# Kernel optimization log

Measured on AMD Instinct MI355X. Metric: run time of the kernel, lower is better.

Reference implementation:

```python
import jax, jax.numpy as jnp
import numpy as np

H = 8          # kv heads
D = 128        # head dim
EPS = 1e-6
NEG = -1e9

def rmsnorm(x, w):
    rms = jnp.sqrt(jnp.mean(x * x, axis=-1, keepdims=True) + EPS)
    return x / rms * w

def apply_rotary(x, cos, sin):
    # x: [B, h, T, D]; cos/sin: [1, 1, T, D/2]
    x1, x2 = jnp.split(x, 2, axis=-1)
    return jnp.concatenate([x1 * cos - x2 * sin, x1 * sin + x2 * cos], axis=-1)


def setup_inputs() -> dict:
    key = jax.random.key(0)
    ks = jax.random.split(key, 7)
    B, T, hid = 1, 4096, 1024
    s = 0.02
    return {
        "x":   jax.random.normal(ks[0], (B, T, hid), jnp.float32),
        "cos": jax.random.normal(ks[1], (1, 1, T, D // 2), jnp.float32),
        "sin": jax.random.normal(ks[2], (1, 1, T, D // 2), jnp.float32),
        "Wq":  jax.random.normal(ks[3], (hid, 2 * hid), jnp.float32) * s,
        "Wk":  jax.random.normal(ks[4], (hid, hid), jnp.float32) * s,
        "Wv":  jax.random.normal(ks[5], (hid, hid), jnp.float32) * s,
        "Wo":  jax.random.normal(ks[6], (2 * hid, hid), jnp.float32) * s,
        "qn_w": jnp.ones((D,), jnp.float32),
        "kn_w": jnp.ones((D,), jnp.float32),
    }


def reference(x, cos, sin, Wq, Wk, Wv, Wo, qn_w, kn_w):
    B, T, _ = x.shape
    scale = D ** -0.5

    q = (x @ Wq).reshape(B, T, 2 * H, D).transpose(0, 2, 1, 3)  # [B,2H,T,D]
    k = (x @ Wk).reshape(B, T, H, D).transpose(0, 2, 1, 3)      # [B,H,T,D]
    v = (x @ Wv).reshape(B, T, H, D).transpose(0, 2, 1, 3)      # [B,H,T,D]

    q = apply_rotary(rmsnorm(q, qn_w), cos, sin)
    k = apply_rotary(rmsnorm(k, kn_w), cos, sin)

    # GQA expand: query head i uses kv head i // 2
    k = jnp.repeat(k, 2, axis=1)  # [B,2H,T,D]
    v = jnp.repeat(v, 2, axis=1)

    attn = jnp.einsum("bhtd,bhsd->bhts", q, k) * scale
    causal = jnp.tril(jnp.ones((T, T), bool))
    attn = jnp.where(causal, attn, NEG)
    attn = jax.nn.softmax(attn, axis=-1)

    out = jnp.einsum("bhts,bhsd->bhtd", attn, v)
    out = out.transpose(0, 2, 1, 3).reshape(B, T, 2 * H * D)
    return out @ Wo
```

## Files before the change

### kernel.cpp

```cpp
#include <hip/hip_runtime.h>
#include <hip/hip_bf16.h>

#define H2 16
#define HKV 8
#define DHEAD 128
#define HID 1024
#define NQ 2048

typedef unsigned short u16;
typedef __bf16 bf16x8 __attribute__((ext_vector_type(8)));
typedef float f32x4 __attribute__((ext_vector_type(4)));

__device__ __forceinline__ u16 f2bf(float x) {
    unsigned int u = __float_as_uint(x);
    unsigned int r = (u + 0x7fffu + ((u >> 16) & 1u)) >> 16;
    return (u16)r;
}
__device__ __forceinline__ float bf2f(u16 x) {
    return __uint_as_float(((unsigned int)x) << 16);
}

__device__ __forceinline__ unsigned int pack_bf16(float hi, float lo) {
    unsigned int a = __float_as_uint(hi) + 0x8000u;
    unsigned int b = __float_as_uint(lo) + 0x8000u;
    return __builtin_amdgcn_perm(a, b, 0x07060302u);
}

__device__ __forceinline__ bf16x8 ld_frag(const u16* p) {
    bf16x8 r;
    *reinterpret_cast<uint4*>(&r) = *reinterpret_cast<const uint4*>(p);
    return r;
}

__device__ __forceinline__ void gload_lds16(const u16* g, u16* l) {
    __builtin_amdgcn_global_load_lds((const __attribute__((address_space(1))) void*)g,
                                     (__attribute__((address_space(3))) void*)l, 16, 0, 0);
}

__global__ __launch_bounds__(256) void cast_f32_bf16(const float* __restrict__ in,
                                                     u16* __restrict__ out, int n4) {
    int i = blockIdx.x * 256 + threadIdx.x;
    if (i < n4) {
        float4 v = reinterpret_cast<const float4*>(in)[i];
        ushort4 o;
        o.x = f2bf(v.x); o.y = f2bf(v.y); o.z = f2bf(v.z); o.w = f2bf(v.w);
        reinterpret_cast<ushort4*>(out)[i] = o;
    }
}

__global__ __launch_bounds__(256) void transpose_cast_all(const float* __restrict__ Wq,
                                                          const float* __restrict__ Wk,
                                                          const float* __restrict__ Wv,
                                                          const float* __restrict__ Wo,
                                                          u16* __restrict__ Wqkvb,
                                                          u16* __restrict__ Wob) {
    __shared__ u16 t[32][34];
    int bid = blockIdx.x;
    const float* in; u16* out; int K, N, k0, n0;
    if (bid < 2048) {
        in = Wq; out = Wqkvb; K = 1024; N = 2048;
        k0 = (bid & 31) * 32; n0 = (bid >> 5) * 32;
    } else if (bid < 3072) {
        int b = bid - 2048;
        in = Wk; out = Wqkvb + (size_t)2048 * 1024; K = 1024; N = 1024;
        k0 = (b & 31) * 32; n0 = (b >> 5) * 32;
    } else if (bid < 4096) {
        int b = bid - 3072;
        in = Wv; out = Wqkvb + (size_t)3072 * 1024; K = 1024; N = 1024;
        k0 = (b & 31) * 32; n0 = (b >> 5) * 32;
    } else {
        int b = bid - 4096;
        in = Wo; out = Wob; K = 2048; N = 1024;
        k0 = (b & 63) * 32; n0 = (b >> 6) * 32;
    }
    for (int c = threadIdx.x; c < 1024; c += 256) {
        int k = c >> 5, n = c & 31;
        t[k][n] = f2bf(in[(size_t)(k0 + k) * N + n0 + n]);
    }
    __syncthreads();
    for (int c = threadIdx.x; c < 1024; c += 256) {
        int n = c >> 5, k = c & 31;
        out[(size_t)(n0 + n) * K + k0 + k] = t[k][n];
    }
}

template <bool OUT_BF16>
__global__ __launch_bounds__(256) void gemm_bf16_t(const u16* __restrict__ A,
                                                   const u16* __restrict__ Bt,
                                                   void* __restrict__ Cv,
                                                   int M, int N, int K) {
    __shared__ u16 As[2][128 * 32];
    __shared__ u16 Bs[2][128 * 32];
    int tid = threadIdx.x;
    int lane = tid & 63, wave = tid >> 6;
    int quad = lane >> 4, l15 = lane & 15;
    int wr = wave >> 1, wc = wave & 1;
    int m0 = blockIdx.y * 128, n0 = blockIdx.x * 128;

    f32x4 zero = {0.f, 0.f, 0.f, 0.f};
    f32x4 acc[4][4];
    for (int i = 0; i < 4; i++)
        for (int j = 0; j < 4; j++) acc[i][j] = zero;

    int r0 = 16 * wave + (lane >> 2);
    int r1 = r0 + 64;
    int ks0 = (lane & 3) ^ ((r0 >> 1) & 3);
    int ks1 = (lane & 3) ^ ((r1 >> 1) & 3);
    const u16* ga0 = A + (size_t)(m0 + r0) * K + ks0 * 8;
    const u16* ga1 = A + (size_t)(m0 + r1) * K + ks1 * 8;
    const u16* gb0 = Bt + (size_t)(n0 + r0) * K + ks0 * 8;
    const u16* gb1 = Bt + (size_t)(n0 + r1) * K + ks1 * 8;

    int swz = (quad ^ ((l15 >> 1) & 3)) * 8;

    for (int k0 = 0; k0 < K; k0 += 64) {
        __syncthreads();
        #pragma unroll
        for (int s = 0; s < 2; s++) {
            gload_lds16(ga0 + k0 + s * 32, &As[s][wave * 512]);
            gload_lds16(ga1 + k0 + s * 32, &As[s][(wave + 4) * 512]);
            gload_lds16(gb0 + k0 + s * 32, &Bs[s][wave * 512]);
            gload_lds16(gb1 + k0 + s * 32, &Bs[s][(wave + 4) * 512]);
        }
        __syncthreads();
        #pragma unroll
        for (int s = 0; s < 2; s++) {
            bf16x8 a[4], b[4];
            #pragma unroll
            for (int i = 0; i < 4; i++) a[i] = ld_frag(&As[s][(64 * wr + 16 * i + l15) * 32 + swz]);
            #pragma unroll
            for (int j = 0; j < 4; j++) b[j] = ld_frag(&Bs[s][(64 * wc + 16 * j + l15) * 32 + swz]);
            #pragma unroll
            for (int i = 0; i < 4; i++)
                #pragma unroll
                for (int j = 0; j < 4; j++)
                    acc[i][j] = __builtin_amdgcn_mfma_f32_16x16x32_bf16(a[i], b[j], acc[i][j], 0, 0, 0);
        }
    }
    for (int i = 0; i < 4; i++) {
        int rowb = m0 + 64 * wr + 16 * i + quad * 4;
        for (int j = 0; j < 4; j++) {
            int col = n0 + 64 * wc + 16 * j + l15;
            for (int r = 0; r < 4; r++) {
                if (OUT_BF16)
                    ((u16*)Cv)[(size_t)(rowb + r) * N + col] = f2bf(acc[i][j][r]);
                else
                    ((float*)Cv)[(size_t)(rowb + r) * N + col] = acc[i][j][r];
            }
        }
    }
}

__global__ __launch_bounds__(256) void gemm_bf16_n64(const u16* __restrict__ A,
                                                     const u16* __restrict__ Bt,
                                                     float* __restrict__ C,
                                                     int M, int N, int K) {
    __shared__ u16 As[2][128 * 32];
    __shared__ u16 Bs[2][64 * 32];
    int tid = threadIdx.x;
    int lane = tid & 63, wave = tid >> 6;
    int quad = lane >> 4, l15 = lane & 15;
    int m0 = blockIdx.y * 128, n0 = blockIdx.x * 64;

    f32x4 zero = {0.f, 0.f, 0.f, 0.f};
    f32x4 acc[2][4];
    for (int i = 0; i < 2; i++)
        for (int j = 0; j < 4; j++) acc[i][j] = zero;

    int ra0 = 32 * wave + (lane >> 2);
    int ra1 = ra0 + 16;
    int rb  = 16 * wave + (lane >> 2);
    int ksa0 = (lane & 3) ^ ((ra0 >> 1) & 3);
    int ksa1 = (lane & 3) ^ ((ra1 >> 1) & 3);
    int ksb  = (lane & 3) ^ ((rb >> 1) & 3);
    const u16* ga0 = A + (size_t)(m0 + ra0) * K + ksa0 * 8;
    const u16* ga1 = A + (size_t)(m0 + ra1) * K + ksa1 * 8;
    const u16* gb  = Bt + (size_t)(n0 + rb) * K + ksb * 8;

    int swz = (quad ^ ((l15 >> 1) & 3)) * 8;

    for (int k0 = 0; k0 < K; k0 += 64) {
        __syncthreads();
        #pragma unroll
        for (int s = 0; s < 2; s++) {
            gload_lds16(ga0 + k0 + s * 32, &As[s][(2 * wave) * 512]);
            gload_lds16(ga1 + k0 + s * 32, &As[s][(2 * wave + 1) * 512]);
            gload_lds16(gb + k0 + s * 32, &Bs[s][wave * 512]);
        }
        __syncthreads();
        #pragma unroll
        for (int s = 0; s < 2; s++) {
            bf16x8 a[2], b[4];
            #pragma unroll
            for (int i = 0; i < 2; i++) a[i] = ld_frag(&As[s][(32 * wave + 16 * i + l15) * 32 + swz]);
            #pragma unroll
            for (int j = 0; j < 4; j++) b[j] = ld_frag(&Bs[s][(16 * j + l15) * 32 + swz]);
            #pragma unroll
            for (int i = 0; i < 2; i++)
                #pragma unroll
                for (int j = 0; j < 4; j++)
                    acc[i][j] = __builtin_amdgcn_mfma_f32_16x16x32_bf16(a[i], b[j], acc[i][j], 0, 0, 0);
        }
    }
    for (int i = 0; i < 2; i++) {
        int rowb = m0 + 32 * wave + 16 * i + quad * 4;
        for (int j = 0; j < 4; j++) {
            int col = n0 + 16 * j + l15;
            for (int r = 0; r < 4; r++)
                C[(size_t)(rowb + r) * N + col] = acc[i][j][r];
        }
    }
}

__global__ __launch_bounds__(256) void norm_rope_qk(const u16* __restrict__ qkv,
                                                    const float* __restrict__ cosp,
                                                    const float* __restrict__ sinp,
                                                    const float* __restrict__ qnw,
                                                    const float* __restrict__ knw,
                                                    u16* __restrict__ Qb,
                                                    u16* __restrict__ Kb,
                                                    int T, float qscale) {
    int wave = threadIdx.x >> 6, lane = threadIdx.x & 63;
    int wid = blockIdx.x * 4 + wave;
    int t = wid / 24, unit = wid % 24;
    if (t >= T) return;
    bool isq = unit < 16;
    int coloff = isq ? unit * 128 : 2048 + (unit - 16) * 128;
    const float* w = isq ? qnw : knw;
    float outscale = isq ? qscale : 1.0f;
    u16* out = isq ? (Qb + ((size_t)unit * T + t) * 128)
                   : (Kb + ((size_t)(unit - 16) * T + t) * 128);
    const u16* r = qkv + (size_t)t * 4096 + coloff;
    float v1 = bf2f(r[lane]), v2 = bf2f(r[lane + 64]);
    float ss = v1 * v1 + v2 * v2;
    for (int off = 1; off < 64; off <<= 1) ss += __shfl_xor(ss, off);
    float inv = rsqrtf(ss * (1.f / 128.f) + 1e-6f);
    float n1 = v1 * inv * w[lane], n2 = v2 * inv * w[lane + 64];
    float c = cosp[(size_t)t * 64 + lane], s = sinp[(size_t)t * 64 + lane];
    float o1 = (n1 * c - n2 * s) * outscale;
    float o2 = (n1 * s + n2 * c) * outscale;
    out[lane] = f2bf(o1);
    out[lane + 64] = f2bf(o2);
}

__global__ __launch_bounds__(256) void v_transpose(const u16* __restrict__ qkv,
                                                   u16* __restrict__ Vbt, int T) {
    __shared__ u16 tt[128][72];
    int h = blockIdx.y, t0 = blockIdx.x * 64;
    for (int c = threadIdx.x; c < 8192; c += 256) {
        int r = c >> 7, d = c & 127;
        tt[d][r] = qkv[(size_t)(t0 + r) * 4096 + 3072 + h * 128 + d];
    }
    __syncthreads();
    for (int c = threadIdx.x; c < 8192; c += 256) {
        int d = c >> 6, r = c & 63;
        Vbt[((size_t)h * 128 + d) * T + t0 + r] = tt[d][r];
    }
}

__global__ __launch_bounds__(512, 4) void flash_attn(const u16* __restrict__ Qb,
                                                     const u16* __restrict__ Kb,
                                                     const u16* __restrict__ Vbt,
                                                     u16* __restrict__ attn, int T) {
    __shared__ u16 Ks[2][64 * 128];
    __shared__ u16 Vt[2][128 * 64];
    __shared__ u16 Ps[64 * 64];
    __shared__ float Ms[4][2][16];
    __shared__ float Ls[4][2][16];
    int tid = threadIdx.x;
    int lane = tid & 63, wave = tid >> 6;
    int qw = wave & 3, sh = wave >> 2;
    int quad = lane >> 4, l15 = lane & 15;
    int swb8 = (l15 & 7) * 8;
    int h = blockIdx.y;
    int j = (int)blockIdx.x;
    int kvh = h >> 1;

    const u16* kbase = Kb + (size_t)kvh * T * 128;
    const u16* vbase = Vbt + (size_t)kvh * 128 * T;

    int krow_ = lane >> 4;
    int kseg_ = lane & 15;
    int vrow_ = lane >> 3;
    int vseg_ = lane & 7;

    auto stage = [&](int s0, int b) {
        #pragma unroll
        for (int i = 0; i < 2; i++) {
            int ch = wave * 2 + i;
            int r = ch * 4 + krow_;
            int s = kseg_ ^ (r & 7);
            gload_lds16(kbase + (size_t)(s0 + r) * 128 + s * 8, &Ks[b][ch * 512]);
        }
        #pragma unroll
        for (int i = 0; i < 2; i++) {
            int ch = wave * 2 + i;
            int d = ch * 8 + vrow_;
            int s = vseg_ ^ (d & 7);
            gload_lds16(vbase + (size_t)d * T + s0 + s * 8, &Vt[b][ch * 512]);
        }
    };

    bf16x8 onesf;
    #pragma unroll
    for (int i = 0; i < 8; i++) onesf[i] = (__bf16)1.0f;
    f32x4 zero = {0.f, 0.f, 0.f, 0.f};
    const float L2E = 1.44269504f;

    for (int pass = 0; pass < 2; ++pass) {
        int qt = pass == 0 ? (63 - j) : j;
        int q0 = qt * 64;

        bf16x8 qf[4];
        {
            const u16* qp = Qb + ((size_t)h * T + q0 + 16 * qw + l15) * 128 + quad * 8;
            #pragma unroll
            for (int kk = 0; kk < 4; kk++) qf[kk] = ld_frag(qp + kk * 32);
        }

        float m_i = -3.0e38f;
        f32x4 lsum = zero;
        f32x4 o[8];
        for (int dt = 0; dt < 8; dt++) o[dt] = zero;

        int ntiles = qt + 1;
        stage(0, 0);
        __syncthreads();

        for (int it = 0; it < ntiles; ++it) {
            int b = it & 1;
            if (it + 1 < ntiles) stage((it + 1) * 64, 1 - b);
            bool diag = (it == qt);
            if (!(diag && sh == 1 && qw < 2)) {
                f32x4 scT[2];
                scT[0] = zero; scT[1] = zero;
                #pragma unroll
                for (int kk = 0; kk < 4; kk++)
                    #pragma unroll
                    for (int jt = 0; jt < 2; jt++) {
                        bf16x8 kfrag = ld_frag(&Ks[b][(sh * 32 + jt * 16 + l15) * 128 + ((kk * 32 + quad * 8) ^ swb8)]);
                        scT[jt] = __builtin_amdgcn_mfma_f32_16x16x32_bf16(kfrag, qf[kk], scT[jt], 0, 0, 0);
                    }

                if (diag) {
                    int qloc = 16 * qw + l15;
                    #pragma unroll
                    for (int jt = 0; jt < 2; jt++)
                        for (int r = 0; r < 4; r++)
                            if (sh * 32 + jt * 16 + quad * 4 + r > qloc) scT[jt][r] = -1e30f;
                }

                float mt = scT[0][0];
                #pragma unroll
                for (int jt = 0; jt < 2; jt++)
                    for (int r = 0; r < 4; r++) mt = fmaxf(mt, scT[jt][r]);
                mt = fmaxf(mt, __shfl_xor(mt, 16));
                mt = fmaxf(mt, __shfl_xor(mt, 32));
                float mnew = fmaxf(m_i, mt);
                float alpha = __expf(m_i - mnew);
                m_i = mnew;
                float mls = mnew * L2E;

                #pragma unroll
                for (int jt = 0; jt < 2; jt++)
                    for (int r = 0; r < 4; r++)
                        scT[jt][r] = exp2f(fmaf(scT[jt][r], L2E, -mls));

                {
                    int prow = 16 * qw + l15;
                    #pragma unroll
                    for (int jt = 0; jt < 2; jt++) {
                        int s8 = sh * 4 + 2 * jt + (quad >> 1);
                        uint2 wv;
                        wv.x = pack_bf16(scT[jt][1], scT[jt][0]);
                        wv.y = pack_bf16(scT[jt][3], scT[jt][2]);
                        *reinterpret_cast<uint2*>(&Ps[prow * 64 + (s8 ^ (l15 & 7)) * 8 + (quad & 1) * 4]) = wv;
                    }
                }

                if (__any(alpha != 1.0f)) {
                    float av[4];
                    #pragma unroll
                    for (int r = 0; r < 4; r++) av[r] = __shfl(alpha, quad * 4 + r);
                    #pragma unroll
                    for (int r = 0; r < 4; r++) lsum[r] *= av[r];
                    #pragma unroll
                    for (int dt = 0; dt < 8; dt++)
                        for (int r = 0; r < 4; r++) o[dt][r] *= av[r];
                }

                asm volatile("s_waitcnt lgkmcnt(0)" ::: "memory");

                bf16x8 pa = ld_frag(&Ps[(16 * qw + l15) * 64 + (((sh * 4 + quad) ^ (l15 & 7)) * 8)]);
                lsum = __builtin_amdgcn_mfma_f32_16x16x32_bf16(pa, onesf, lsum, 0, 0, 0);
                #pragma unroll
                for (int dt = 0; dt < 8; dt++) {
                    bf16x8 vb = ld_frag(&Vt[b][(dt * 16 + l15) * 64 + (((sh * 4 + quad) * 8) ^ swb8)]);
                    o[dt] = __builtin_amdgcn_mfma_f32_16x16x32_bf16(pa, vb, o[dt], 0, 0, 0);
                }
            }
            __syncthreads();
        }

        if (quad == 0) Ms[qw][sh][l15] = m_i;
        if (l15 == 0) {
            #pragma unroll
            for (int r = 0; r < 4; r++) Ls[qw][sh][quad * 4 + r] = lsum[r];
        }
        __syncthreads();
        float M4[4], wS[4];
        #pragma unroll
        for (int r = 0; r < 4; r++) {
            float mS = Ms[qw][sh][quad * 4 + r];
            float mO = Ms[qw][sh ^ 1][quad * 4 + r];
            M4[r] = fmaxf(mS, mO);
            wS[r] = __expf(mS - M4[r]);
        }
        float* scr = reinterpret_cast<float*>(&Ks[0][0]);
        if (sh == 1) {
            #pragma unroll
            for (int dt = 0; dt < 8; dt++)
                #pragma unroll
                for (int r = 0; r < 4; r++)
                    scr[qw * 2048 + (dt * 16 + l15) * 16 + ((quad * 4 + r) ^ l15)] = o[dt][r] * wS[r];
        }
        __syncthreads();
        if (sh == 0) {
            float inv[4];
            #pragma unroll
            for (int r = 0; r < 4; r++) {
                float mO = Ms[qw][1][quad * 4 + r];
                float wO = __expf(mO - M4[r]);
                float l = lsum[r] * wS[r] + Ls[qw][1][quad * 4 + r] * wO;
                inv[r] = 1.f / l;
            }
            #pragma unroll
            for (int dt = 0; dt < 8; dt++)
                #pragma unroll
                for (int r = 0; r < 4; r++) {
                    float val = (o[dt][r] * wS[r] +
                                 scr[qw * 2048 + (dt * 16 + l15) * 16 + ((quad * 4 + r) ^ l15)]) * inv[r];
                    int row = q0 + 16 * qw + quad * 4 + r;
                    attn[(size_t)row * NQ + h * DHEAD + dt * 16 + l15] = f2bf(val);
                }
        }
        __syncthreads();
    }
}

extern "C" void kernel_launch(void* const* d_in, const int* in_sizes, int n_in,
                              void* d_out, int out_size, void* d_ws, size_t ws_size,
                              hipStream_t stream) {
    const float* x    = (const float*)d_in[0];
    const float* cosp = (const float*)d_in[1];
    const float* sinp = (const float*)d_in[2];
    const float* Wq   = (const float*)d_in[3];
    const float* Wk   = (const float*)d_in[4];
    const float* Wv   = (const float*)d_in[5];
    const float* Wo   = (const float*)d_in[6];
    const float* qnw  = (const float*)d_in[7];
    const float* knw  = (const float*)d_in[8];
    float* out = (float*)d_out;
    const int T = in_sizes[1] / 64;

    char* ws = (char*)d_ws;
    size_t off = 0;
    auto alloc = [&](size_t bytes) {
        char* p = ws + off;
        off += (bytes + 255) & ~(size_t)255;
        return p;
    };
    u16*   xb     = (u16*)alloc((size_t)T * HID * 2);
    u16*   Wqkvb  = (u16*)alloc((size_t)4096 * HID * 2);
    u16*   Wob    = (u16*)alloc((size_t)HID * NQ * 2);
    u16*   qkvb   = (u16*)alloc((size_t)T * 4096 * 2);
    u16*   Qb     = (u16*)alloc((size_t)H2 * T * DHEAD * 2);
    u16*   Kb     = (u16*)alloc((size_t)HKV * T * DHEAD * 2);
    u16*   Vbt    = (u16*)alloc((size_t)HKV * DHEAD * T * 2);
    u16*   attn   = (u16*)alloc((size_t)T * NQ * 2);

    cast_f32_bf16<<<(T * HID / 4 + 255) / 256, 256, 0, stream>>>(x, xb, T * HID / 4);
    transpose_cast_all<<<6144, 256, 0, stream>>>(Wq, Wk, Wv, Wo, Wqkvb, Wob);

    gemm_bf16_t<true><<<dim3(4096 / 128, T / 128), 256, 0, stream>>>(xb, Wqkvb, qkvb, T, 4096, HID);

    const float scale = 0.08838834764831845f;
    norm_rope_qk<<<T * 24 / 4, 256, 0, stream>>>(qkvb, cosp, sinp, qnw, knw, Qb, Kb, T, scale);
    v_transpose<<<dim3(T / 64, HKV), 256, 0, stream>>>(qkvb, Vbt, T);

    flash_attn<<<dim3(32, H2), 512, 0, stream>>>(Qb, Kb, Vbt, attn, T);

    gemm_bf16_n64<<<dim3(HID / 64, T / 128), 256, 0, stream>>>(attn, Wob, out, T, HID, NQ);
}
```

Baseline: 354.3 us.

## Enlarge flash attention query tile to 128 rows per block

Each block now handles 128 query rows instead of 64, with each wave computing two 16-row query sub-tiles against the same K/V fragments. This doubles the reuse of every K and V tile staged into shared memory and halves the number of blocks. In exchange, register pressure roughly doubles (launch bounds drop to 2 blocks per CU), the grid shrinks to 256 blocks, and causal masking now runs over a two-tile diagonal zone.

```diff
diff --git a/kernel.cpp b/kernel.cpp
--- a/kernel.cpp
+++ b/kernel.cpp
@@ -258,22 +258,23 @@
     }
 }
 
-__global__ __launch_bounds__(512, 4) void flash_attn(const u16* __restrict__ Qb,
+__global__ __launch_bounds__(512, 2) void flash_attn(const u16* __restrict__ Qb,
                                                      const u16* __restrict__ Kb,
                                                      const u16* __restrict__ Vbt,
                                                      u16* __restrict__ attn, int T) {
     __shared__ u16 Ks[2][64 * 128];
     __shared__ u16 Vt[2][128 * 64];
-    __shared__ u16 Ps[64 * 64];
-    __shared__ float Ms[4][2][16];
-    __shared__ float Ls[4][2][16];
+    __shared__ u16 Ps[128 * 64];
+    __shared__ float Ms[4][2][32];
+    __shared__ float Ls[4][2][32];
     int tid = threadIdx.x;
     int lane = tid & 63, wave = tid >> 6;
     int qw = wave & 3, sh = wave >> 2;
     int quad = lane >> 4, l15 = lane & 15;
     int swb8 = (l15 & 7) * 8;
     int h = blockIdx.y;
-    int j = (int)blockIdx.x;
+    int jj = (int)blockIdx.x;
+    int nqt = T >> 7;
     int kvh = h >> 1;
 
     const u16* kbase = Kb + (size_t)kvh * T * 128;
@@ -308,141 +309,171 @@
     const float L2E = 1.44269504f;
 
     for (int pass = 0; pass < 2; ++pass) {
-        int qt = pass == 0 ? (63 - j) : j;
-        int q0 = qt * 64;
-
-        bf16x8 qf[4];
-        {
-            const u16* qp = Qb + ((size_t)h * T + q0 + 16 * qw + l15) * 128 + quad * 8;
-            #pragma unroll
-            for (int kk = 0; kk < 4; kk++) qf[kk] = ld_frag(qp + kk * 32);
-        }
-
-        float m_i = -3.0e38f;
-        f32x4 lsum = zero;
-        f32x4 o[8];
-        for (int dt = 0; dt < 8; dt++) o[dt] = zero;
-
-        int ntiles = qt + 1;
+        int qt = pass == 0 ? (nqt - 1 - jj) : jj;
+        int q0 = qt * 128;
+
+        bf16x8 qf[2][4];
+        #pragma unroll
+        for (int qs = 0; qs < 2; qs++) {
+            const u16* qp = Qb + ((size_t)h * T + q0 + 32 * qw + 16 * qs + l15) * 128 + quad * 8;
+            #pragma unroll
+            for (int kk = 0; kk < 4; kk++) qf[qs][kk] = ld_frag(qp + kk * 32);
+        }
+
+        float m_i[2] = {-3.0e38f, -3.0e38f};
+        f32x4 lsum[2] = {zero, zero};
+        f32x4 o[2][8];
+        #pragma unroll
+        for (int qs = 0; qs < 2; qs++)
+            #pragma unroll
+            for (int dt = 0; dt < 8; dt++) o[qs][dt] = zero;
+
+        int ntiles = 2 * qt + 2;
         stage(0, 0);
         __syncthreads();
 
         for (int it = 0; it < ntiles; ++it) {
             int b = it & 1;
             if (it + 1 < ntiles) stage((it + 1) * 64, 1 - b);
-            bool diag = (it == qt);
-            if (!(diag && sh == 1 && qw < 2)) {
-                f32x4 scT[2];
-                scT[0] = zero; scT[1] = zero;
+            bool diagzone = (it >= 2 * qt);
+            int sbl = (it - 2 * qt) * 64 + 32 * sh;
+            bool skip = diagzone && (32 * qw + 31 < sbl);
+            if (!skip) {
+                f32x4 scT[2][2];
+                scT[0][0] = zero; scT[0][1] = zero; scT[1][0] = zero; scT[1][1] = zero;
                 #pragma unroll
                 for (int kk = 0; kk < 4; kk++)
                     #pragma unroll
                     for (int jt = 0; jt < 2; jt++) {
-                        bf16x8 kfrag = ld_frag(&Ks[b][(sh * 32 + jt * 16 + l15) * 128 + ((kk * 32 + quad * 8) ^ swb8)]);
-                        scT[jt] = __builtin_amdgcn_mfma_f32_16x16x32_bf16(kfrag, qf[kk], scT[jt], 0, 0, 0);
+                        bf16x8 kfrag = ld_frag(&Ks[b][(32 * sh + 16 * jt + l15) * 128 + ((kk * 32 + quad * 8) ^ swb8)]);
+                        scT[0][jt] = __builtin_amdgcn_mfma_f32_16x16x32_bf16(kfrag, qf[0][kk], scT[0][jt], 0, 0, 0);
+                        scT[1][jt] = __builtin_amdgcn_mfma_f32_16x16x32_bf16(kfrag, qf[1][kk], scT[1][jt], 0, 0, 0);
                     }
 
-                if (diag) {
-                    int qloc = 16 * qw + l15;
+                if (diagzone) {
+                    #pragma unroll
+                    for (int qs = 0; qs < 2; qs++) {
+                        int qloc = 32 * qw + 16 * qs + l15;
+                        #pragma unroll
+                        for (int jt = 0; jt < 2; jt++)
+                            for (int r = 0; r < 4; r++)
+                                if (sbl + 16 * jt + quad * 4 + r > qloc) scT[qs][jt][r] = -1e30f;
+                    }
+                }
+
+                #pragma unroll
+                for (int qs = 0; qs < 2; qs++) {
+                    float mt = scT[qs][0][0];
+                    #pragma unroll
+                    for (int jt = 0; jt < 2; jt++)
+                        for (int r = 0; r < 4; r++) mt = fmaxf(mt, scT[qs][jt][r]);
+                    mt = fmaxf(mt, __shfl_xor(mt, 16));
+                    mt = fmaxf(mt, __shfl_xor(mt, 32));
+                    float mnew = fmaxf(m_i[qs], mt);
+                    float alpha = __expf(m_i[qs] - mnew);
+                    m_i[qs] = mnew;
+                    float mls = mnew * L2E;
+
                     #pragma unroll
                     for (int jt = 0; jt < 2; jt++)
                         for (int r = 0; r < 4; r++)
-                            if (sh * 32 + jt * 16 + quad * 4 + r > qloc) scT[jt][r] = -1e30f;
-                }
-
-                float mt = scT[0][0];
-                #pragma unroll
-                for (int jt = 0; jt < 2; jt++)
-                    for (int r = 0; r < 4; r++) mt = fmaxf(mt, scT[jt][r]);
-                mt = fmaxf(mt, __shfl_xor(mt, 16));
-                mt = fmaxf(mt, __shfl_xor(mt, 32));
-                float mnew = fmaxf(m_i, mt);
-                float alpha = __expf(m_i - mnew);
-                m_i = mnew;
-                float mls = mnew * L2E;
-
-                #pragma unroll
-                for (int jt = 0; jt < 2; jt++)
-                    for (int r = 0; r < 4; r++)
-                        scT[jt][r] = exp2f(fmaf(scT[jt][r], L2E, -mls));
-
-                {
-                    int prow = 16 * qw + l15;
-                    #pragma unroll
-                    for (int jt = 0; jt < 2; jt++) {
-                        int s8 = sh * 4 + 2 * jt + (quad >> 1);
-                        uint2 wv;
-                        wv.x = pack_bf16(scT[jt][1], scT[jt][0]);
-                        wv.y = pack_bf16(scT[jt][3], scT[jt][2]);
-                        *reinterpret_cast<uint2*>(&Ps[prow * 64 + (s8 ^ (l15 & 7)) * 8 + (quad & 1) * 4]) = wv;
+                            scT[qs][jt][r] = exp2f(fmaf(scT[qs][jt][r], L2E, -mls));
+
+                    {
+                        int prow = 32 * qw + 16 * qs + l15;
+                        #pragma unroll
+                        for (int jt = 0; jt < 2; jt++) {
+                            int s8 = sh * 4 + 2 * jt + (quad >> 1);
+                            uint2 wv;
+                            wv.x = pack_bf16(scT[qs][jt][1], scT[qs][jt][0]);
+                            wv.y = pack_bf16(scT[qs][jt][3], scT[qs][jt][2]);
+                            *reinterpret_cast<uint2*>(&Ps[prow * 64 + (s8 ^ (l15 & 7)) * 8 + (quad & 1) * 4]) = wv;
+                        }
+                    }
+
+                    if (__any(alpha != 1.0f)) {
+                        float av[4];
+                        #pragma unroll
+                        for (int r = 0; r < 4; r++) av[r] = __shfl(alpha, quad * 4 + r);
+                        #pragma unroll
+                        for (int r = 0; r < 4; r++) lsum[qs][r] *= av[r];
+                        #pragma unroll
+                        for (int dt = 0; dt < 8; dt++)
+                            for (int r = 0; r < 4; r++) o[qs][dt][r] *= av[r];
                     }
                 }
 
-                if (__any(alpha != 1.0f)) {
-                    float av[4];
-                    #pragma unroll
-                    for (int r = 0; r < 4; r++) av[r] = __shfl(alpha, quad * 4 + r);
-                    #pragma unroll
-                    for (int r = 0; r < 4; r++) lsum[r] *= av[r];
-                    #pragma unroll
-                    for (int dt = 0; dt < 8; dt++)
-                        for (int r = 0; r < 4; r++) o[dt][r] *= av[r];
-                }
-
                 asm volatile("s_waitcnt lgkmcnt(0)" ::: "memory");
 
-                bf16x8 pa = ld_frag(&Ps[(16 * qw + l15) * 64 + (((sh * 4 + quad) ^ (l15 & 7)) * 8)]);
-                lsum = __builtin_amdgcn_mfma_f32_16x16x32_bf16(pa, onesf, lsum, 0, 0, 0);
+                bf16x8 pa0 = ld_frag(&Ps[(32 * qw + l15) * 64 + (((sh * 4 + quad) ^ (l15 & 7)) * 8)]);
+                bf16x8 pa1 = ld_frag(&Ps[(32 * qw + 16 + l15) * 64 + (((sh * 4 + quad) ^ (l15 & 7)) * 8)]);
+                lsum[0] = __builtin_amdgcn_mfma_f32_16x16x32_bf16(pa0, onesf, lsum[0], 0, 0, 0);
+                lsum[1] = __builtin_amdgcn_mfma_f32_16x16x32_bf16(pa1, onesf, lsum[1], 0, 0, 0);
                 #pragma unroll
                 for (int dt = 0; dt < 8; dt++) {
                     bf16x8 vb = ld_frag(&Vt[b][(dt * 16 + l15) * 64 + (((sh * 4 + quad) * 8) ^ swb8)]);
-                    o[dt] = __builtin_amdgcn_mfma_f32_16x16x32_bf16(pa, vb, o[dt], 0, 0, 0);
+                    o[0][dt] = __builtin_amdgcn_mfma_f32_16x16x32_bf16(pa0, vb, o[0][dt], 0, 0, 0);
+                    o[1][dt] = __builtin_amdgcn_mfma_f32_16x16x32_bf16(pa1, vb, o[1][dt], 0, 0, 0);
                 }
             }
             __syncthreads();
         }
 
-        if (quad == 0) Ms[qw][sh][l15] = m_i;
+        if (quad == 0) { Ms[qw][sh][l15] = m_i[0]; Ms[qw][sh][16 + l15] = m_i[1]; }
         if (l15 == 0) {
             #pragma unroll
-            for (int r = 0; r < 4; r++) Ls[qw][sh][quad * 4 + r] = lsum[r];
-        }
-        __syncthreads();
-        float M4[4], wS[4];
-        #pragma unroll
-        for (int r = 0; r < 4; r++) {
-            float mS = Ms[qw][sh][quad * 4 + r];
-            float mO = Ms[qw][sh ^ 1][quad * 4 + r];
-            M4[r] = fmaxf(mS, mO);
-            wS[r] = __expf(mS - M4[r]);
-        }
-        float* scr = reinterpret_cast<float*>(&Ks[0][0]);
+            for (int qs = 0; qs < 2; qs++)
+                for (int r = 0; r < 4; r++) Ls[qw][sh][16 * qs + quad * 4 + r] = lsum[qs][r];
+        }
+        __syncthreads();
+        float M4[2][4], wS[2][4];
+        #pragma unroll
+        for (int qs = 0; qs < 2; qs++)
+            for (int r = 0; r < 4; r++) {
+                int qidx = 16 * qs + quad * 4 + r;
+                float mS = Ms[qw][sh][qidx];
+                float mO = Ms[qw][sh ^ 1][qidx];
+                M4[qs][r] = fmaxf(mS, mO);
+                wS[qs][r] = __expf(mS - M4[qs][r]);
+            }
+        float* scr = (qw < 2) ? reinterpret_cast<float*>(&Ks[0][0]) + qw * 4096
+                              : reinterpret_cast<float*>(&Vt[0][0]) + (qw - 2) * 4096;
         if (sh == 1) {
             #pragma unroll
-            for (int dt = 0; dt < 8; dt++)
-                #pragma unroll
-                for (int r = 0; r < 4; r++)
-                    scr[qw * 2048 + (dt * 16 + l15) * 16 + ((quad * 4 + r) ^ l15)] = o[dt][r] * wS[r];
+            for (int dt = 0; dt < 8; dt++) {
+                int d = dt * 16 + l15;
+                #pragma unroll
+                for (int qs = 0; qs < 2; qs++)
+                    for (int r = 0; r < 4; r++) {
+                        int qp_ = 16 * qs + quad * 4 + r;
+                        scr[d * 32 + (qp_ ^ (d & 31))] = o[qs][dt][r] * wS[qs][r];
+                    }
+            }
         }
         __syncthreads();
         if (sh == 0) {
-            float inv[4];
-            #pragma unroll
-            for (int r = 0; r < 4; r++) {
-                float mO = Ms[qw][1][quad * 4 + r];
-                float wO = __expf(mO - M4[r]);
-                float l = lsum[r] * wS[r] + Ls[qw][1][quad * 4 + r] * wO;
-                inv[r] = 1.f / l;
+            float inv[2][4];
+            #pragma unroll
+            for (int qs = 0; qs < 2; qs++)
+                for (int r = 0; r < 4; r++) {
+                    int qidx = 16 * qs + quad * 4 + r;
+                    float mO = Ms[qw][1][qidx];
+                    float wO = __expf(mO - M4[qs][r]);
+                    float l = lsum[qs][r] * wS[qs][r] + Ls[qw][1][qidx] * wO;
+                    inv[qs][r] = 1.f / l;
+                }
+            #pragma unroll
+            for (int dt = 0; dt < 8; dt++) {
+                int d = dt * 16 + l15;
+                #pragma unroll
+                for (int qs = 0; qs < 2; qs++)
+                    for (int r = 0; r < 4; r++) {
+                        int qp_ = 16 * qs + quad * 4 + r;
+                        float val = (o[qs][dt][r] * wS[qs][r] + scr[d * 32 + (qp_ ^ (d & 31))]) * inv[qs][r];
+                        int row = q0 + 32 * qw + qp_;
+                        attn[(size_t)row * NQ + h * DHEAD + d] = f2bf(val);
+                    }
             }
-            #pragma unroll
-            for (int dt = 0; dt < 8; dt++)
-                #pragma unroll
-                for (int r = 0; r < 4; r++) {
-                    float val = (o[dt][r] * wS[r] +
-                                 scr[qw * 2048 + (dt * 16 + l15) * 16 + ((quad * 4 + r) ^ l15)]) * inv[r];
-                    int row = q0 + 16 * qw + quad * 4 + r;
-                    attn[(size_t)row * NQ + h * DHEAD + dt * 16 + l15] = f2bf(val);
-                }
         }
         __syncthreads();
     }
@@ -488,7 +519,7 @@
     norm_rope_qk<<<T * 24 / 4, 256, 0, stream>>>(qkvb, cosp, sinp, qnw, knw, Qb, Kb, T, scale);
     v_transpose<<<dim3(T / 64, HKV), 256, 0, stream>>>(qkvb, Vbt, T);
 
-    flash_attn<<<dim3(32, H2), 512, 0, stream>>>(Qb, Kb, Vbt, attn, T);
+    flash_attn<<<dim3(T / 256, H2), 512, 0, stream>>>(Qb, Kb, Vbt, attn, T);
 
     gemm_bf16_n64<<<dim3(HID / 64, T / 128), 256, 0, stream>>>(attn, Wob, out, T, HID, NQ);
 }
```

After: 345.3 us. -2.6%, faster.

## Software-pipeline QK^T of next tile with softmax/PV of current tile

Applied to the files above, without the earlier changes.

Splits K and V staging so K is prefetched two tiles ahead. The QK^T MFMAs for the next tile are issued between the softmax exponentials and the PV MFMAs of the current tile, so matrix and vector work can overlap. This costs extra live registers for the second score accumulator and an extra prologue sync, which may lower occupancy.

```diff
diff --git a/kernel.cpp b/kernel.cpp
--- a/kernel.cpp
+++ b/kernel.cpp
@@ -284,7 +284,7 @@
     int vrow_ = lane >> 3;
     int vseg_ = lane & 7;
 
-    auto stage = [&](int s0, int b) {
+    auto stageK = [&](int s0, int b) {
         #pragma unroll
         for (int i = 0; i < 2; i++) {
             int ch = wave * 2 + i;
@@ -292,6 +292,8 @@
             int s = kseg_ ^ (r & 7);
             gload_lds16(kbase + (size_t)(s0 + r) * 128 + s * 8, &Ks[b][ch * 512]);
         }
+    };
+    auto stageV = [&](int s0, int b) {
         #pragma unroll
         for (int i = 0; i < 2; i++) {
             int ch = wave * 2 + i;
@@ -318,30 +320,42 @@
             for (int kk = 0; kk < 4; kk++) qf[kk] = ld_frag(qp + kk * 32);
         }
 
+        auto computeQK = [&](f32x4* sc, int kb) {
+            sc[0] = zero; sc[1] = zero;
+            #pragma unroll
+            for (int kk = 0; kk < 4; kk++)
+                #pragma unroll
+                for (int jt = 0; jt < 2; jt++) {
+                    bf16x8 kfrag = ld_frag(&Ks[kb][(sh * 32 + jt * 16 + l15) * 128 + ((kk * 32 + quad * 8) ^ swb8)]);
+                    sc[jt] = __builtin_amdgcn_mfma_f32_16x16x32_bf16(kfrag, qf[kk], sc[jt], 0, 0, 0);
+                }
+        };
+
         float m_i = -3.0e38f;
         f32x4 lsum = zero;
         f32x4 o[8];
         for (int dt = 0; dt < 8; dt++) o[dt] = zero;
 
         int ntiles = qt + 1;
-        stage(0, 0);
+        stageK(0, 0);
+        stageV(0, 0);
+        if (ntiles > 1) stageK(64, 1);
+        __syncthreads();
+
+        f32x4 scT[2];
+        computeQK(scT, 0);
         __syncthreads();
 
         for (int it = 0; it < ntiles; ++it) {
             int b = it & 1;
-            if (it + 1 < ntiles) stage((it + 1) * 64, 1 - b);
+            if (it + 2 < ntiles) stageK((it + 2) * 64, b);
+            if (it + 1 < ntiles) stageV((it + 1) * 64, 1 - b);
+
             bool diag = (it == qt);
-            if (!(diag && sh == 1 && qw < 2)) {
-                f32x4 scT[2];
-                scT[0] = zero; scT[1] = zero;
-                #pragma unroll
-                for (int kk = 0; kk < 4; kk++)
-                    #pragma unroll
-                    for (int jt = 0; jt < 2; jt++) {
-                        bf16x8 kfrag = ld_frag(&Ks[b][(sh * 32 + jt * 16 + l15) * 128 + ((kk * 32 + quad * 8) ^ swb8)]);
-                        scT[jt] = __builtin_amdgcn_mfma_f32_16x16x32_bf16(kfrag, qf[kk], scT[jt], 0, 0, 0);
-                    }
-
+            bool skip = diag && sh == 1 && qw < 2;
+            float alpha = 1.0f;
+
+            if (!skip) {
                 if (diag) {
                     int qloc = 16 * qw + l15;
                     #pragma unroll
@@ -357,7 +371,7 @@
                 mt = fmaxf(mt, __shfl_xor(mt, 16));
                 mt = fmaxf(mt, __shfl_xor(mt, 32));
                 float mnew = fmaxf(m_i, mt);
-                float alpha = __expf(m_i - mnew);
+                alpha = __expf(m_i - mnew);
                 m_i = mnew;
                 float mls = mnew * L2E;
 
@@ -365,7 +379,12 @@
                 for (int jt = 0; jt < 2; jt++)
                     for (int r = 0; r < 4; r++)
                         scT[jt][r] = exp2f(fmaf(scT[jt][r], L2E, -mls));
-
+            }
+
+            f32x4 scN[2];
+            if (it + 1 < ntiles) computeQK(scN, 1 - b);
+
+            if (!skip) {
                 {
                     int prow = 16 * qw + l15;
                     #pragma unroll
@@ -400,6 +419,7 @@
                 }
             }
             __syncthreads();
+            if (it + 1 < ntiles) { scT[0] = scN[0]; scT[1] = scN[1]; }
         }
 
         if (quad == 0) Ms[qw][sh][l15] = m_i;
```

Result: slower. 362.1 us (+2.2%).

## Fuse RMSNorm, RoPE and V transpose into QKV GEMM epilogue

Applied to the files above, without the earlier changes.

The QKV projection GEMM now stages its 128x128 output tile in shared memory with an XOR swizzle. Its epilogue applies RMSNorm and rotary embedding for Q/K head tiles, or writes the transposed V tile directly. This removes the intermediate qkv buffer round trip through global memory and two extra kernel launches. In exchange the epilogue is serialized per wave, handling 32 rows each with shuffle reductions, which lengthens the GEMM tail.

```diff
diff --git a/kernel.cpp b/kernel.cpp
--- a/kernel.cpp
+++ b/kernel.cpp
@@ -84,13 +84,20 @@
     }
 }
 
-template <bool OUT_BF16>
-__global__ __launch_bounds__(256) void gemm_bf16_t(const u16* __restrict__ A,
-                                                   const u16* __restrict__ Bt,
-                                                   void* __restrict__ Cv,
-                                                   int M, int N, int K) {
-    __shared__ u16 As[2][128 * 32];
-    __shared__ u16 Bs[2][128 * 32];
+__global__ __launch_bounds__(256) void gemm_qkv_fused(const u16* __restrict__ A,
+                                                      const u16* __restrict__ Bt,
+                                                      const float* __restrict__ cosp,
+                                                      const float* __restrict__ sinp,
+                                                      const float* __restrict__ qnw,
+                                                      const float* __restrict__ knw,
+                                                      u16* __restrict__ Qb,
+                                                      u16* __restrict__ Kb,
+                                                      u16* __restrict__ Vbt,
+                                                      int T, float qscale) {
+    __shared__ u16 smem[16384];
+    u16* Asm = smem;
+    u16* Bsm = smem + 8192;
+    const int K = 1024, N = 4096;
     int tid = threadIdx.x;
     int lane = tid & 63, wave = tid >> 6;
     int quad = lane >> 4, l15 = lane & 15;
@@ -117,19 +124,19 @@
         __syncthreads();
         #pragma unroll
         for (int s = 0; s < 2; s++) {
-            gload_lds16(ga0 + k0 + s * 32, &As[s][wave * 512]);
-            gload_lds16(ga1 + k0 + s * 32, &As[s][(wave + 4) * 512]);
-            gload_lds16(gb0 + k0 + s * 32, &Bs[s][wave * 512]);
-            gload_lds16(gb1 + k0 + s * 32, &Bs[s][(wave + 4) * 512]);
+            gload_lds16(ga0 + k0 + s * 32, &Asm[s * 4096 + wave * 512]);
+            gload_lds16(ga1 + k0 + s * 32, &Asm[s * 4096 + (wave + 4) * 512]);
+            gload_lds16(gb0 + k0 + s * 32, &Bsm[s * 4096 + wave * 512]);
+            gload_lds16(gb1 + k0 + s * 32, &Bsm[s * 4096 + (wave + 4) * 512]);
         }
         __syncthreads();
         #pragma unroll
         for (int s = 0; s < 2; s++) {
             bf16x8 a[4], b[4];
             #pragma unroll
-            for (int i = 0; i < 4; i++) a[i] = ld_frag(&As[s][(64 * wr + 16 * i + l15) * 32 + swz]);
-            #pragma unroll
-            for (int j = 0; j < 4; j++) b[j] = ld_frag(&Bs[s][(64 * wc + 16 * j + l15) * 32 + swz]);
+            for (int i = 0; i < 4; i++) a[i] = ld_frag(&Asm[s * 4096 + (64 * wr + 16 * i + l15) * 32 + swz]);
+            #pragma unroll
+            for (int j = 0; j < 4; j++) b[j] = ld_frag(&Bsm[s * 4096 + (64 * wc + 16 * j + l15) * 32 + swz]);
             #pragma unroll
             for (int i = 0; i < 4; i++)
                 #pragma unroll
@@ -137,16 +144,54 @@
                     acc[i][j] = __builtin_amdgcn_mfma_f32_16x16x32_bf16(a[i], b[j], acc[i][j], 0, 0, 0);
         }
     }
+
+    __syncthreads();
+    u16* Ct = smem;
+    #pragma unroll
     for (int i = 0; i < 4; i++) {
-        int rowb = m0 + 64 * wr + 16 * i + quad * 4;
+        int rowb = 64 * wr + 16 * i + quad * 4;
+        #pragma unroll
         for (int j = 0; j < 4; j++) {
-            int col = n0 + 64 * wc + 16 * j + l15;
+            int col = 64 * wc + 16 * j + l15;
+            #pragma unroll
             for (int r = 0; r < 4; r++) {
-                if (OUT_BF16)
-                    ((u16*)Cv)[(size_t)(rowb + r) * N + col] = f2bf(acc[i][j][r]);
-                else
-                    ((float*)Cv)[(size_t)(rowb + r) * N + col] = acc[i][j][r];
+                int row = rowb + r;
+                Ct[row * 128 + (col ^ (row & 63))] = f2bf(acc[i][j][r]);
             }
+        }
+    }
+    __syncthreads();
+
+    if (n0 < 3072) {
+        bool isq = n0 < 2048;
+        int hh = isq ? (n0 >> 7) : ((n0 - 2048) >> 7);
+        const float* w = isq ? qnw : knw;
+        float outscale = isq ? qscale : 1.0f;
+        u16* outp = isq ? (Qb + (size_t)hh * T * 128) : (Kb + (size_t)hh * T * 128);
+        int d = lane;
+        float wd1 = w[d], wd2 = w[d + 64];
+        for (int rr = 0; rr < 32; rr++) {
+            int row = wave * 32 + rr;
+            int t = m0 + row;
+            float v1 = bf2f(Ct[row * 128 + (d ^ (row & 63))]);
+            float v2 = bf2f(Ct[row * 128 + ((d + 64) ^ (row & 63))]);
+            float ss = v1 * v1 + v2 * v2;
+            for (int off = 1; off < 64; off <<= 1) ss += __shfl_xor(ss, off);
+            float inv = rsqrtf(ss * (1.f / 128.f) + 1e-6f);
+            float n1 = v1 * inv * wd1, n2 = v2 * inv * wd2;
+            float c = cosp[(size_t)t * 64 + d], s = sinp[(size_t)t * 64 + d];
+            u16* orow = outp + (size_t)t * 128;
+            orow[d] = f2bf((n1 * c - n2 * s) * outscale);
+            orow[d + 64] = f2bf((n1 * s + n2 * c) * outscale);
+        }
+    } else {
+        int vh = (n0 - 3072) >> 7;
+        for (int dd = 0; dd < 32; dd++) {
+            int dcol = wave * 32 + dd;
+            u16* vrow = Vbt + ((size_t)vh * 128 + dcol) * T + m0;
+            int t1 = lane, t2 = lane + 64;
+            vrow[t1] = Ct[t1 * 128 + (dcol ^ (t1 & 63))];
+            vrow[t2] = Ct[t2 * 128 + (dcol ^ (t2 & 63))];
         }
     }
 }
@@ -209,52 +254,6 @@
             for (int r = 0; r < 4; r++)
                 C[(size_t)(rowb + r) * N + col] = acc[i][j][r];
         }
-    }
-}
-
-__global__ __launch_bounds__(256) void norm_rope_qk(const u16* __restrict__ qkv,
-                                                    const float* __restrict__ cosp,
-                                                    const float* __restrict__ sinp,
-                                                    const float* __restrict__ qnw,
-                                                    const float* __restrict__ knw,
-                                                    u16* __restrict__ Qb,
-                                                    u16* __restrict__ Kb,
-                                                    int T, float qscale) {
-    int wave = threadIdx.x >> 6, lane = threadIdx.x & 63;
-    int wid = blockIdx.x * 4 + wave;
-    int t = wid / 24, unit = wid % 24;
-    if (t >= T) return;
-    bool isq = unit < 16;
-    int coloff = isq ? unit * 128 : 2048 + (unit - 16) * 128;
-    const float* w = isq ? qnw : knw;
-    float outscale = isq ? qscale : 1.0f;
-    u16* out = isq ? (Qb + ((size_t)unit * T + t) * 128)
-                   : (Kb + ((size_t)(unit - 16) * T + t) * 128);
-    const u16* r = qkv + (size_t)t * 4096 + coloff;
-    float v1 = bf2f(r[lane]), v2 = bf2f(r[lane + 64]);
-    float ss = v1 * v1 + v2 * v2;
-    for (int off = 1; off < 64; off <<= 1) ss += __shfl_xor(ss, off);
-    float inv = rsqrtf(ss * (1.f / 128.f) + 1e-6f);
-    float n1 = v1 * inv * w[lane], n2 = v2 * inv * w[lane + 64];
-    float c = cosp[(size_t)t * 64 + lane], s = sinp[(size_t)t * 64 + lane];
-    float o1 = (n1 * c - n2 * s) * outscale;
-    float o2 = (n1 * s + n2 * c) * outscale;
-    out[lane] = f2bf(o1);
-    out[lane + 64] = f2bf(o2);
-}
-
-__global__ __launch_bounds__(256) void v_transpose(const u16* __restrict__ qkv,
-                                                   u16* __restrict__ Vbt, int T) {
-    __shared__ u16 tt[128][72];
-    int h = blockIdx.y, t0 = blockIdx.x * 64;
-    for (int c = threadIdx.x; c < 8192; c += 256) {
-        int r = c >> 7, d = c & 127;
-        tt[d][r] = qkv[(size_t)(t0 + r) * 4096 + 3072 + h * 128 + d];
-    }
-    __syncthreads();
-    for (int c = threadIdx.x; c < 8192; c += 256) {
-        int d = c >> 6, r = c & 63;
-        Vbt[((size_t)h * 128 + d) * T + t0 + r] = tt[d][r];
     }
 }
 
@@ -473,7 +472,6 @@
     u16*   xb     = (u16*)alloc((size_t)T * HID * 2);
     u16*   Wqkvb  = (u16*)alloc((size_t)4096 * HID * 2);
     u16*   Wob    = (u16*)alloc((size_t)HID * NQ * 2);
-    u16*   qkvb   = (u16*)alloc((size_t)T * 4096 * 2);
     u16*   Qb     = (u16*)alloc((size_t)H2 * T * DHEAD * 2);
     u16*   Kb     = (u16*)alloc((size_t)HKV * T * DHEAD * 2);
     u16*   Vbt    = (u16*)alloc((size_t)HKV * DHEAD * T * 2);
@@ -482,11 +480,9 @@
     cast_f32_bf16<<<(T * HID / 4 + 255) / 256, 256, 0, stream>>>(x, xb, T * HID / 4);
     transpose_cast_all<<<6144, 256, 0, stream>>>(Wq, Wk, Wv, Wo, Wqkvb, Wob);
 
-    gemm_bf16_t<true><<<dim3(4096 / 128, T / 128), 256, 0, stream>>>(xb, Wqkvb, qkvb, T, 4096, HID);
-
     const float scale = 0.08838834764831845f;
-    norm_rope_qk<<<T * 24 / 4, 256, 0, stream>>>(qkvb, cosp, sinp, qnw, knw, Qb, Kb, T, scale);
-    v_transpose<<<dim3(T / 64, HKV), 256, 0, stream>>>(qkvb, Vbt, T);
+    gemm_qkv_fused<<<dim3(4096 / 128, T / 128), 256, 0, stream>>>(
+        xb, Wqkvb, cosp, sinp, qnw, knw, Qb, Kb, Vbt, T, scale);
 
     flash_attn<<<dim3(32, H2), 512, 0, stream>>>(Qb, Kb, Vbt, attn, T);
 
```

New measurement: 343.1 us. 1.03x faster.
